# Performance work log

Measured on AMD Instinct MI355X. Metric: run time of the kernel, lower is better.

## Reference

```python
import jax, jax.numpy as jnp
import numpy as np

MARGIN = 0.1  # init kwarg


def setup_inputs() -> dict:
    key = jax.random.key(0)
    k1, k2, k3 = jax.random.split(key, 3)
    B, P, D = 256, 64, 1024
    imFtr = jax.random.normal(k1, (B, P, D), dtype=jnp.float32)
    disFtr = jax.random.normal(k2, (B, D), dtype=jnp.float32)
    lblList = jax.random.randint(k3, (B,), 0, 100000, dtype=jnp.int64 if jax.config.read('jax_enable_x64') else jnp.int32)
    return {"imFtr": imFtr, "disFtr": disFtr, "lblList": lblList}


def reference(imFtr, disFtr, lblList):
    B, P, D = imFtr.shape
    # simMM: [B*P, B] -> [B, P, B]; max over proposals P -> simMax [B, B]
    simMM = jnp.einsum('bpd,cd->bpc', imFtr, disFtr)
    simMax = jnp.max(simMM, axis=1)  # [B, B] (rows: image/video i, cols: text j)
    pos = jnp.diagonal(simMax)       # [B]

    # valid negative pairs: labels differ (diagonal excluded automatically)
    mask = (lblList[:, None] != lblList[None, :]).astype(simMax.dtype)  # [B, B]
    pairNum = jnp.sum(mask)

    # image -> text ranking: relu(sim[i, j] - sim[i, i] + margin)
    loss_it = jnp.sum(jnp.maximum(simMax - pos[:, None] + MARGIN, 0.0) * mask)
    loss = loss_it / pairNum

    # biLossFlag: text -> image ranking: relu(sim[j, i] - sim[i, i] + margin)
    loss_ti = jnp.sum(jnp.maximum(simMax - pos[None, :] + MARGIN, 0.0) * mask)
    loss = loss + jnp.where(pairNum > 0, loss_ti / pairNum, 0.0)

    return loss.reshape(1)
```

## Files before the change

### kernel.cpp

```cpp
#include <hip/hip_runtime.h>

constexpr int NB = 256;
constexpr int NP = 64;
constexpr int ND = 1024;
constexpr float MARGIN = 0.1f;

typedef __attribute__((ext_vector_type(8))) short bf16x8;
typedef __attribute__((ext_vector_type(4))) short bf16x4;
typedef __attribute__((ext_vector_type(4))) float f32x4;

static __device__ inline unsigned short f2bf(float f) {
  unsigned u = __builtin_bit_cast(unsigned, f);
  u += 0x7fffu + ((u >> 16) & 1u);
  return (unsigned short)(u >> 16);
}

static __device__ inline bf16x8 cvt8(float4 a, float4 b) {
  bf16x8 r;
  r[0] = (short)f2bf(a.x); r[1] = (short)f2bf(a.y);
  r[2] = (short)f2bf(a.z); r[3] = (short)f2bf(a.w);
  r[4] = (short)f2bf(b.x); r[5] = (short)f2bf(b.y);
  r[6] = (short)f2bf(b.z); r[7] = (short)f2bf(b.w);
  return r;
}

static __device__ inline bf16x4 cvt4(float4 a) {
  bf16x4 r;
  r[0] = (short)f2bf(a.x); r[1] = (short)f2bf(a.y);
  r[2] = (short)f2bf(a.z); r[3] = (short)f2bf(a.w);
  return r;
}

__global__ __launch_bounds__(256) void cvtB_kernel(
    const float* __restrict__ src, short* __restrict__ dst) {
  const int idx = (blockIdx.x * 256 + threadIdx.x) * 4;
  float4 v = *reinterpret_cast<const float4*>(src + idx);
  *reinterpret_cast<bf16x4*>(dst + idx) = cvt4(v);
}

__global__ __launch_bounds__(1024, 4) void simmax_kernel(
    const float* __restrict__ imFtr, const short* __restrict__ disB,
    float* __restrict__ simMax) {
  const int i  = blockIdx.x;
  const int t  = threadIdx.x;
  const int w  = t >> 6;
  const int l  = t & 63;
  const int lr = l & 15;
  const int lk = l >> 4;

  __shared__ short Asl[2][NP][256];

  f32x4 acc[4];
#pragma unroll
  for (int pt = 0; pt < 4; ++pt)
#pragma unroll
    for (int r = 0; r < 4; ++r) acc[pt][r] = 0.0f;

  const int ar = t >> 4;
  const int aj = t & 15;
  const float* abase = imFtr + ((size_t)i * NP + ar) * ND + aj * 4;
  float4 areg[4];

  const short* bp = disB + (size_t)(w * 16 + lr) * ND + lk * 8;
  bf16x8 breg[8];

#define STAGE_LOAD(C)                                                        \
  _Pragma("unroll")                                                          \
  for (int g = 0; g < 4; ++g)                                                \
    areg[g] = *reinterpret_cast<const float4*>(abase + (C) * 256 + g * 64);

#define STAGE_WRITE(BUF)                                                     \
  _Pragma("unroll")                                                          \
  for (int g = 0; g < 4; ++g) {                                              \
    const int s  = g * 8 + (aj >> 1);                                        \
    const int so = (s ^ (ar & 15)) * 8 + (aj & 1) * 4;                       \
    *reinterpret_cast<bf16x4*>(&Asl[BUF][ar][so]) = cvt4(areg[g]);           \
  }

  STAGE_LOAD(0);
#pragma unroll
  for (int j = 0; j < 8; ++j)
    breg[j] = *reinterpret_cast<const bf16x8*>(bp + j * 32);
  STAGE_WRITE(0);
  __syncthreads();

#pragma unroll
  for (int c = 0; c < 4; ++c) {
    const int cb = c & 1;
    if (c < 3) STAGE_LOAD(c + 1);
#pragma unroll
    for (int j8 = 0; j8 < 8; ++j8) {
      const int jj = c * 8 + j8;
      const int so = ((j8 * 4 + lk) ^ lr) * 8;
      bf16x8 a0 = *reinterpret_cast<const bf16x8*>(&Asl[cb][lr][so]);
      bf16x8 a1 = *reinterpret_cast<const bf16x8*>(&Asl[cb][16 + lr][so]);
      bf16x8 a2 = *reinterpret_cast<const bf16x8*>(&Asl[cb][32 + lr][so]);
      bf16x8 a3 = *reinterpret_cast<const bf16x8*>(&Asl[cb][48 + lr][so]);
      acc[0] = __builtin_amdgcn_mfma_f32_16x16x32_bf16(a0, breg[j8], acc[0], 0, 0, 0);
      acc[1] = __builtin_amdgcn_mfma_f32_16x16x32_bf16(a1, breg[j8], acc[1], 0, 0, 0);
      acc[2] = __builtin_amdgcn_mfma_f32_16x16x32_bf16(a2, breg[j8], acc[2], 0, 0, 0);
      acc[3] = __builtin_amdgcn_mfma_f32_16x16x32_bf16(a3, breg[j8], acc[3], 0, 0, 0);
      if (jj + 8 < 32)
        breg[j8] = *reinterpret_cast<const bf16x8*>(bp + (jj + 8) * 32);
    }
    if (c < 3) {
      STAGE_WRITE(cb ^ 1);
      __syncthreads();
    }
  }

#undef STAGE_LOAD
#undef STAGE_WRITE

  float m = acc[0][0];
#pragma unroll
  for (int pt = 0; pt < 4; ++pt)
#pragma unroll
    for (int r = 0; r < 4; ++r) m = fmaxf(m, acc[pt][r]);
  m = fmaxf(m, __shfl_xor(m, 16));
  m = fmaxf(m, __shfl_xor(m, 32));
  if (l < 16) simMax[(size_t)i * NB + w * 16 + lr] = m;
}

__global__ __launch_bounds__(512) void simmax_fallback_kernel(
    const float* __restrict__ imFtr, const float* __restrict__ disFtr,
    float* __restrict__ simMax) {
  const int i  = blockIdx.x;
  const int t  = threadIdx.x;
  const int w  = t >> 6;
  const int l  = t & 63;
  const int lr = l & 15;
  const int lk = l >> 4;

  __shared__ short Asl[NP][64];

  f32x4 acc[4][2];
#pragma unroll
  for (int pt = 0; pt < 4; ++pt)
#pragma unroll
    for (int ct = 0; ct < 2; ++ct)
#pragma unroll
      for (int r = 0; r < 4; ++r) acc[pt][ct][r] = 0.0f;

  const int ar  = t >> 3;
  const int aks = t & 7;
  const float* ap = imFtr + (size_t)i * NP * ND + (size_t)ar * ND + aks * 8;
  const int wslot = ((aks ^ (ar & 7)) * 8);
  float4 av0 = *reinterpret_cast<const float4*>(ap);
  float4 av1 = *reinterpret_cast<const float4*>(ap + 4);

  const float* bp0 = disFtr + (size_t)(w * 32 + lr) * ND + lk * 8;
  const float* bp1 = disFtr + (size_t)(w * 32 + 16 + lr) * ND + lk * 8;

  for (int kc = 0; kc < 16; ++kc) {
    const int kbase = kc * 64;
    float4 bld[2][2][2];
#pragma unroll
    for (int ks = 0; ks < 2; ++ks) {
      const int ko = kbase + ks * 32;
      bld[ks][0][0] = *reinterpret_cast<const float4*>(bp0 + ko);
      bld[ks][0][1] = *reinterpret_cast<const float4*>(bp0 + ko + 4);
      bld[ks][1][0] = *reinterpret_cast<const float4*>(bp1 + ko);
      bld[ks][1][1] = *reinterpret_cast<const float4*>(bp1 + ko + 4);
    }
    __syncthreads();
    *reinterpret_cast<bf16x8*>(&Asl[ar][wslot]) = cvt8(av0, av1);
    if (kc < 15) {
      const float* apn = ap + (kc + 1) * 64;
      av0 = *reinterpret_cast<const float4*>(apn);
      av1 = *reinterpret_cast<const float4*>(apn + 4);
    }
    __syncthreads();

#pragma unroll
    for (int ks = 0; ks < 2; ++ks) {
      bf16x8 bfr0 = cvt8(bld[ks][0][0], bld[ks][0][1]);
      bf16x8 bfr1 = cvt8(bld[ks][1][0], bld[ks][1][1]);
#pragma unroll
      for (int pt = 0; pt < 4; ++pt) {
        const int row  = pt * 16 + lr;
        const int slot = (((ks * 4 + lk) ^ (row & 7)) * 8);
        bf16x8 afr = *reinterpret_cast<const bf16x8*>(&Asl[row][slot]);
        acc[pt][0] = __builtin_amdgcn_mfma_f32_16x16x32_bf16(afr, bfr0, acc[pt][0], 0, 0, 0);
        acc[pt][1] = __builtin_amdgcn_mfma_f32_16x16x32_bf16(afr, bfr1, acc[pt][1], 0, 0, 0);
      }
    }
  }

#pragma unroll
  for (int ct = 0; ct < 2; ++ct) {
    float m = acc[0][ct][0];
#pragma unroll
    for (int pt = 0; pt < 4; ++pt)
#pragma unroll
      for (int r = 0; r < 4; ++r) m = fmaxf(m, acc[pt][ct][r]);
    m = fmaxf(m, __shfl_xor(m, 16));
    m = fmaxf(m, __shfl_xor(m, 32));
    if (l < 16) simMax[(size_t)i * NB + w * 32 + ct * 16 + l] = m;
  }
}

__global__ __launch_bounds__(256) void loss_kernel(
    const float* __restrict__ simMax, const int* __restrict__ lbl,
    float* __restrict__ partial) {
  const int i = blockIdx.x;
  const int j = threadIdx.x;
  __shared__ float posi_sh;
  __shared__ float red[3][4];

  float s = simMax[(size_t)i * NB + j];
  if (j == i) posi_sh = s;
  __syncthreads();
  const float posi = posi_sh;
  const float posj = simMax[(size_t)j * NB + j];

  const float msk = (lbl[i] != lbl[j]) ? 1.0f : 0.0f;
  float c  = msk;
  float l1 = msk * fmaxf(s - posi + MARGIN, 0.0f);
  float l2 = msk * fmaxf(s - posj + MARGIN, 0.0f);
#pragma unroll
  for (int o = 32; o > 0; o >>= 1) {
    c  += __shfl_down(c, o);
    l1 += __shfl_down(l1, o);
    l2 += __shfl_down(l2, o);
  }
  const int w = j >> 6;
  if ((j & 63) == 0) { red[0][w] = c; red[1][w] = l1; red[2][w] = l2; }
  __syncthreads();
  if (j == 0) {
    partial[i * 3 + 0] = red[0][0] + red[0][1] + red[0][2] + red[0][3];
    partial[i * 3 + 1] = red[1][0] + red[1][1] + red[1][2] + red[1][3];
    partial[i * 3 + 2] = red[2][0] + red[2][1] + red[2][2] + red[2][3];
  }
}

__global__ __launch_bounds__(256) void finalize_kernel(
    const float* __restrict__ partial, float* __restrict__ out) {
  const int t = threadIdx.x;
  __shared__ float red[3][4];
  float c  = partial[t * 3 + 0];
  float l1 = partial[t * 3 + 1];
  float l2 = partial[t * 3 + 2];
#pragma unroll
  for (int o = 32; o > 0; o >>= 1) {
    c  += __shfl_down(c, o);
    l1 += __shfl_down(l1, o);
    l2 += __shfl_down(l2, o);
  }
  const int w = t >> 6;
  if ((t & 63) == 0) { red[0][w] = c; red[1][w] = l1; red[2][w] = l2; }
  __syncthreads();
  if (t == 0) {
    float cs  = red[0][0] + red[0][1] + red[0][2] + red[0][3];
    float l1s = red[1][0] + red[1][1] + red[1][2] + red[1][3];
    float l2s = red[2][0] + red[2][1] + red[2][2] + red[2][3];
    float loss = l1s / cs;
    loss += (cs > 0.0f) ? (l2s / cs) : 0.0f;
    out[0] = loss;
  }
}

extern "C" void kernel_launch(void* const* d_in, const int* in_sizes, int n_in,
                              void* d_out, int out_size, void* d_ws, size_t ws_size,
                              hipStream_t stream) {
  (void)in_sizes; (void)n_in; (void)out_size;
  const float* imFtr  = (const float*)d_in[0];
  const float* disFtr = (const float*)d_in[1];
  const int*   lbl    = (const int*)d_in[2];
  float* out = (float*)d_out;

  const size_t disB_bytes = (size_t)NB * ND * sizeof(short);
  const size_t sim_bytes  = (size_t)NB * NB * sizeof(float);
  const size_t need = disB_bytes + sim_bytes + 3 * NB * sizeof(float);

  if (ws_size >= need) {
    short* disB    = (short*)d_ws;
    float* simMax  = (float*)((char*)d_ws + disB_bytes);
    float* partial = (float*)((char*)d_ws + disB_bytes + sim_bytes);

    cvtB_kernel<<<dim3(NB), dim3(256), 0, stream>>>(disFtr, disB);
    simmax_kernel<<<dim3(NB), dim3(1024), 0, stream>>>(imFtr, disB, simMax);
    loss_kernel<<<dim3(NB), dim3(256), 0, stream>>>(simMax, lbl, partial);
    finalize_kernel<<<dim3(1), dim3(256), 0, stream>>>(partial, out);
  } else {
    float* simMax  = (float*)d_ws;
    float* partial = (float*)((char*)d_ws + (size_t)NB * NB * 4);
    simmax_fallback_kernel<<<dim3(NB), dim3(512), 0, stream>>>(imFtr, disFtr, simMax);
    loss_kernel<<<dim3(NB), dim3(256), 0, stream>>>(simMax, lbl, partial);
    finalize_kernel<<<dim3(1), dim3(256), 0, stream>>>(partial, out);
  }
}
```

Before: 34.48 us.

## Fuse conversion, simMax GEMM and loss reductions into one cooperative kernel

Replaces four separate launches (bf16 conversion, simMax GEMM, per-row loss, finalize) with a single cooperative kernel that uses grid.sync between phases. The goal is to remove launch gaps and kernel boundaries on a short pipeline. In exchange it adds three grid-wide barriers and depends on all 256 blocks of 1024 threads being co-resident. It also drops the workspace-size fallback path. The first A-tile prefetch is issued before the conversion phase so its latency overlaps the first barrier.

```diff
diff --git a/kernel.cpp b/kernel.cpp
--- a/kernel.cpp
+++ b/kernel.cpp
@@ -1,4 +1,7 @@
 #include <hip/hip_runtime.h>
+#include <hip/hip_cooperative_groups.h>
+
+namespace cg = cooperative_groups;
 
 constexpr int NB = 256;
 constexpr int NP = 64;
@@ -13,15 +16,6 @@
   unsigned u = __builtin_bit_cast(unsigned, f);
   u += 0x7fffu + ((u >> 16) & 1u);
   return (unsigned short)(u >> 16);
-}
-
-static __device__ inline bf16x8 cvt8(float4 a, float4 b) {
-  bf16x8 r;
-  r[0] = (short)f2bf(a.x); r[1] = (short)f2bf(a.y);
-  r[2] = (short)f2bf(a.z); r[3] = (short)f2bf(a.w);
-  r[4] = (short)f2bf(b.x); r[5] = (short)f2bf(b.y);
-  r[6] = (short)f2bf(b.z); r[7] = (short)f2bf(b.w);
-  return r;
 }
 
 static __device__ inline bf16x4 cvt4(float4 a) {
@@ -31,16 +25,13 @@
   return r;
 }
 
-__global__ __launch_bounds__(256) void cvtB_kernel(
-    const float* __restrict__ src, short* __restrict__ dst) {
-  const int idx = (blockIdx.x * 256 + threadIdx.x) * 4;
-  float4 v = *reinterpret_cast<const float4*>(src + idx);
-  *reinterpret_cast<bf16x4*>(dst + idx) = cvt4(v);
-}
-
-__global__ __launch_bounds__(1024, 4) void simmax_kernel(
-    const float* __restrict__ imFtr, const short* __restrict__ disB,
-    float* __restrict__ simMax) {
+__global__ __launch_bounds__(1024, 4) void fused_kernel(
+    const float* __restrict__ imFtr, const float* __restrict__ disFtr,
+    const int* __restrict__ lbl, float* __restrict__ out,
+    short* __restrict__ disB, float* __restrict__ simMax,
+    float* __restrict__ partial) {
+  cg::grid_group grid = cg::this_grid();
+
   const int i  = blockIdx.x;
   const int t  = threadIdx.x;
   const int w  = t >> 6;
@@ -49,20 +40,13 @@
   const int lk = l >> 4;
 
   __shared__ short Asl[2][NP][256];
-
-  f32x4 acc[4];
-#pragma unroll
-  for (int pt = 0; pt < 4; ++pt)
-#pragma unroll
-    for (int r = 0; r < 4; ++r) acc[pt][r] = 0.0f;
+  __shared__ float red_sh[3][4];
+  __shared__ float posi_sh;
 
   const int ar = t >> 4;
   const int aj = t & 15;
   const float* abase = imFtr + ((size_t)i * NP + ar) * ND + aj * 4;
   float4 areg[4];
-
-  const short* bp = disB + (size_t)(w * 16 + lr) * ND + lk * 8;
-  bf16x8 breg[8];
 
 #define STAGE_LOAD(C)                                                        \
   _Pragma("unroll")                                                          \
@@ -78,192 +62,137 @@
   }
 
   STAGE_LOAD(0);
-#pragma unroll
-  for (int j = 0; j < 8; ++j)
-    breg[j] = *reinterpret_cast<const bf16x8*>(bp + j * 32);
-  STAGE_WRITE(0);
-  __syncthreads();
-
-#pragma unroll
-  for (int c = 0; c < 4; ++c) {
-    const int cb = c & 1;
-    if (c < 3) STAGE_LOAD(c + 1);
-#pragma unroll
-    for (int j8 = 0; j8 < 8; ++j8) {
-      const int jj = c * 8 + j8;
-      const int so = ((j8 * 4 + lk) ^ lr) * 8;
-      bf16x8 a0 = *reinterpret_cast<const bf16x8*>(&Asl[cb][lr][so]);
-      bf16x8 a1 = *reinterpret_cast<const bf16x8*>(&Asl[cb][16 + lr][so]);
-      bf16x8 a2 = *reinterpret_cast<const bf16x8*>(&Asl[cb][32 + lr][so]);
-      bf16x8 a3 = *reinterpret_cast<const bf16x8*>(&Asl[cb][48 + lr][so]);
-      acc[0] = __builtin_amdgcn_mfma_f32_16x16x32_bf16(a0, breg[j8], acc[0], 0, 0, 0);
-      acc[1] = __builtin_amdgcn_mfma_f32_16x16x32_bf16(a1, breg[j8], acc[1], 0, 0, 0);
-      acc[2] = __builtin_amdgcn_mfma_f32_16x16x32_bf16(a2, breg[j8], acc[2], 0, 0, 0);
-      acc[3] = __builtin_amdgcn_mfma_f32_16x16x32_bf16(a3, breg[j8], acc[3], 0, 0, 0);
-      if (jj + 8 < 32)
-        breg[j8] = *reinterpret_cast<const bf16x8*>(bp + (jj + 8) * 32);
-    }
-    if (c < 3) {
-      STAGE_WRITE(cb ^ 1);
-      __syncthreads();
-    }
-  }
-
+  {
+    const int gid = i * 1024 + t;
+    if (gid < (NB * ND) / 4) {
+      const int idx = gid * 4;
+      float4 v = *reinterpret_cast<const float4*>(disFtr + idx);
+      *reinterpret_cast<bf16x4*>(disB + idx) = cvt4(v);
+    }
+  }
+  grid.sync();
+
+  {
+    f32x4 acc[4];
+#pragma unroll
+    for (int pt = 0; pt < 4; ++pt)
+#pragma unroll
+      for (int r = 0; r < 4; ++r) acc[pt][r] = 0.0f;
+
+    const short* bp = disB + (size_t)(w * 16 + lr) * ND + lk * 8;
+    bf16x8 breg[8];
+#pragma unroll
+    for (int j = 0; j < 8; ++j)
+      breg[j] = *reinterpret_cast<const bf16x8*>(bp + j * 32);
+
+    STAGE_WRITE(0);
+    __syncthreads();
+
+#pragma unroll
+    for (int c = 0; c < 4; ++c) {
+      const int cb = c & 1;
+      if (c < 3) STAGE_LOAD(c + 1);
+#pragma unroll
+      for (int j8 = 0; j8 < 8; ++j8) {
+        const int jj = c * 8 + j8;
+        const int so = ((j8 * 4 + lk) ^ lr) * 8;
+        bf16x8 a0 = *reinterpret_cast<const bf16x8*>(&Asl[cb][lr][so]);
+        bf16x8 a1 = *reinterpret_cast<const bf16x8*>(&Asl[cb][16 + lr][so]);
+        bf16x8 a2 = *reinterpret_cast<const bf16x8*>(&Asl[cb][32 + lr][so]);
+        bf16x8 a3 = *reinterpret_cast<const bf16x8*>(&Asl[cb][48 + lr][so]);
+        acc[0] = __builtin_amdgcn_mfma_f32_16x16x32_bf16(a0, breg[j8], acc[0], 0, 0, 0);
+        acc[1] = __builtin_amdgcn_mfma_f32_16x16x32_bf16(a1, breg[j8], acc[1], 0, 0, 0);
+        acc[2] = __builtin_amdgcn_mfma_f32_16x16x32_bf16(a2, breg[j8], acc[2], 0, 0, 0);
+        acc[3] = __builtin_amdgcn_mfma_f32_16x16x32_bf16(a3, breg[j8], acc[3], 0, 0, 0);
+        if (jj + 8 < 32)
+          breg[j8] = *reinterpret_cast<const bf16x8*>(bp + (jj + 8) * 32);
+      }
+      if (c < 3) {
+        STAGE_WRITE(cb ^ 1);
+        __syncthreads();
+      }
+    }
+
+    float m = acc[0][0];
+#pragma unroll
+    for (int pt = 0; pt < 4; ++pt)
+#pragma unroll
+      for (int r = 0; r < 4; ++r) m = fmaxf(m, acc[pt][r]);
+    m = fmaxf(m, __shfl_xor(m, 16));
+    m = fmaxf(m, __shfl_xor(m, 32));
+    if (l < 16) simMax[(size_t)i * NB + w * 16 + lr] = m;
+  }
 #undef STAGE_LOAD
 #undef STAGE_WRITE
-
-  float m = acc[0][0];
-#pragma unroll
-  for (int pt = 0; pt < 4; ++pt)
-#pragma unroll
-    for (int r = 0; r < 4; ++r) m = fmaxf(m, acc[pt][r]);
-  m = fmaxf(m, __shfl_xor(m, 16));
-  m = fmaxf(m, __shfl_xor(m, 32));
-  if (l < 16) simMax[(size_t)i * NB + w * 16 + lr] = m;
-}
-
-__global__ __launch_bounds__(512) void simmax_fallback_kernel(
-    const float* __restrict__ imFtr, const float* __restrict__ disFtr,
-    float* __restrict__ simMax) {
-  const int i  = blockIdx.x;
-  const int t  = threadIdx.x;
-  const int w  = t >> 6;
-  const int l  = t & 63;
-  const int lr = l & 15;
-  const int lk = l >> 4;
-
-  __shared__ short Asl[NP][64];
-
-  f32x4 acc[4][2];
-#pragma unroll
-  for (int pt = 0; pt < 4; ++pt)
-#pragma unroll
-    for (int ct = 0; ct < 2; ++ct)
-#pragma unroll
-      for (int r = 0; r < 4; ++r) acc[pt][ct][r] = 0.0f;
-
-  const int ar  = t >> 3;
-  const int aks = t & 7;
-  const float* ap = imFtr + (size_t)i * NP * ND + (size_t)ar * ND + aks * 8;
-  const int wslot = ((aks ^ (ar & 7)) * 8);
-  float4 av0 = *reinterpret_cast<const float4*>(ap);
-  float4 av1 = *reinterpret_cast<const float4*>(ap + 4);
-
-  const float* bp0 = disFtr + (size_t)(w * 32 + lr) * ND + lk * 8;
-  const float* bp1 = disFtr + (size_t)(w * 32 + 16 + lr) * ND + lk * 8;
-
-  for (int kc = 0; kc < 16; ++kc) {
-    const int kbase = kc * 64;
-    float4 bld[2][2][2];
-#pragma unroll
-    for (int ks = 0; ks < 2; ++ks) {
-      const int ko = kbase + ks * 32;
-      bld[ks][0][0] = *reinterpret_cast<const float4*>(bp0 + ko);
-      bld[ks][0][1] = *reinterpret_cast<const float4*>(bp0 + ko + 4);
-      bld[ks][1][0] = *reinterpret_cast<const float4*>(bp1 + ko);
-      bld[ks][1][1] = *reinterpret_cast<const float4*>(bp1 + ko + 4);
-    }
-    __syncthreads();
-    *reinterpret_cast<bf16x8*>(&Asl[ar][wslot]) = cvt8(av0, av1);
-    if (kc < 15) {
-      const float* apn = ap + (kc + 1) * 64;
-      av0 = *reinterpret_cast<const float4*>(apn);
-      av1 = *reinterpret_cast<const float4*>(apn + 4);
-    }
-    __syncthreads();
-
-#pragma unroll
-    for (int ks = 0; ks < 2; ++ks) {
-      bf16x8 bfr0 = cvt8(bld[ks][0][0], bld[ks][0][1]);
-      bf16x8 bfr1 = cvt8(bld[ks][1][0], bld[ks][1][1]);
-#pragma unroll
-      for (int pt = 0; pt < 4; ++pt) {
-        const int row  = pt * 16 + lr;
-        const int slot = (((ks * 4 + lk) ^ (row & 7)) * 8);
-        bf16x8 afr = *reinterpret_cast<const bf16x8*>(&Asl[row][slot]);
-        acc[pt][0] = __builtin_amdgcn_mfma_f32_16x16x32_bf16(afr, bfr0, acc[pt][0], 0, 0, 0);
-        acc[pt][1] = __builtin_amdgcn_mfma_f32_16x16x32_bf16(afr, bfr1, acc[pt][1], 0, 0, 0);
-      }
-    }
-  }
-
-#pragma unroll
-  for (int ct = 0; ct < 2; ++ct) {
-    float m = acc[0][ct][0];
-#pragma unroll
-    for (int pt = 0; pt < 4; ++pt)
-#pragma unroll
-      for (int r = 0; r < 4; ++r) m = fmaxf(m, acc[pt][ct][r]);
-    m = fmaxf(m, __shfl_xor(m, 16));
-    m = fmaxf(m, __shfl_xor(m, 32));
-    if (l < 16) simMax[(size_t)i * NB + w * 32 + ct * 16 + l] = m;
-  }
-}
-
-__global__ __launch_bounds__(256) void loss_kernel(
-    const float* __restrict__ simMax, const int* __restrict__ lbl,
-    float* __restrict__ partial) {
-  const int i = blockIdx.x;
-  const int j = threadIdx.x;
-  __shared__ float posi_sh;
-  __shared__ float red[3][4];
-
-  float s = simMax[(size_t)i * NB + j];
-  if (j == i) posi_sh = s;
-  __syncthreads();
-  const float posi = posi_sh;
-  const float posj = simMax[(size_t)j * NB + j];
-
-  const float msk = (lbl[i] != lbl[j]) ? 1.0f : 0.0f;
-  float c  = msk;
-  float l1 = msk * fmaxf(s - posi + MARGIN, 0.0f);
-  float l2 = msk * fmaxf(s - posj + MARGIN, 0.0f);
-#pragma unroll
-  for (int o = 32; o > 0; o >>= 1) {
-    c  += __shfl_down(c, o);
-    l1 += __shfl_down(l1, o);
-    l2 += __shfl_down(l2, o);
-  }
-  const int w = j >> 6;
-  if ((j & 63) == 0) { red[0][w] = c; red[1][w] = l1; red[2][w] = l2; }
-  __syncthreads();
-  if (j == 0) {
-    partial[i * 3 + 0] = red[0][0] + red[0][1] + red[0][2] + red[0][3];
-    partial[i * 3 + 1] = red[1][0] + red[1][1] + red[1][2] + red[1][3];
-    partial[i * 3 + 2] = red[2][0] + red[2][1] + red[2][2] + red[2][3];
-  }
-}
-
-__global__ __launch_bounds__(256) void finalize_kernel(
-    const float* __restrict__ partial, float* __restrict__ out) {
-  const int t = threadIdx.x;
-  __shared__ float red[3][4];
-  float c  = partial[t * 3 + 0];
-  float l1 = partial[t * 3 + 1];
-  float l2 = partial[t * 3 + 2];
-#pragma unroll
-  for (int o = 32; o > 0; o >>= 1) {
-    c  += __shfl_down(c, o);
-    l1 += __shfl_down(l1, o);
-    l2 += __shfl_down(l2, o);
-  }
-  const int w = t >> 6;
-  if ((t & 63) == 0) { red[0][w] = c; red[1][w] = l1; red[2][w] = l2; }
-  __syncthreads();
-  if (t == 0) {
-    float cs  = red[0][0] + red[0][1] + red[0][2] + red[0][3];
-    float l1s = red[1][0] + red[1][1] + red[1][2] + red[1][3];
-    float l2s = red[2][0] + red[2][1] + red[2][2] + red[2][3];
-    float loss = l1s / cs;
-    loss += (cs > 0.0f) ? (l2s / cs) : 0.0f;
-    out[0] = loss;
+  grid.sync();
+
+  {
+    const int j = t;
+    float s = 0.0f, posj = 0.0f, msk = 0.0f;
+    if (j < NB) {
+      s = simMax[(size_t)i * NB + j];
+      if (j == i) posi_sh = s;
+      posj = simMax[(size_t)j * NB + j];
+      msk = (lbl[i] != lbl[j]) ? 1.0f : 0.0f;
+    }
+    __syncthreads();
+    float c = 0.0f, l1 = 0.0f, l2 = 0.0f;
+    if (j < NB) {
+      const float posi = posi_sh;
+      c  = msk;
+      l1 = msk * fmaxf(s - posi + MARGIN, 0.0f);
+      l2 = msk * fmaxf(s - posj + MARGIN, 0.0f);
+    }
+#pragma unroll
+    for (int o = 32; o > 0; o >>= 1) {
+      c  += __shfl_down(c, o);
+      l1 += __shfl_down(l1, o);
+      l2 += __shfl_down(l2, o);
+    }
+    if (j < NB && (j & 63) == 0) {
+      red_sh[0][j >> 6] = c; red_sh[1][j >> 6] = l1; red_sh[2][j >> 6] = l2;
+    }
+    __syncthreads();
+    if (j == 0) {
+      partial[i * 3 + 0] = red_sh[0][0] + red_sh[0][1] + red_sh[0][2] + red_sh[0][3];
+      partial[i * 3 + 1] = red_sh[1][0] + red_sh[1][1] + red_sh[1][2] + red_sh[1][3];
+      partial[i * 3 + 2] = red_sh[2][0] + red_sh[2][1] + red_sh[2][2] + red_sh[2][3];
+    }
+  }
+  grid.sync();
+
+  if (i == 0) {
+    float c = 0.0f, l1 = 0.0f, l2 = 0.0f;
+    if (t < NB) {
+      c  = partial[t * 3 + 0];
+      l1 = partial[t * 3 + 1];
+      l2 = partial[t * 3 + 2];
+    }
+#pragma unroll
+    for (int o = 32; o > 0; o >>= 1) {
+      c  += __shfl_down(c, o);
+      l1 += __shfl_down(l1, o);
+      l2 += __shfl_down(l2, o);
+    }
+    if (t < NB && (t & 63) == 0) {
+      red_sh[0][t >> 6] = c; red_sh[1][t >> 6] = l1; red_sh[2][t >> 6] = l2;
+    }
+    __syncthreads();
+    if (t == 0) {
+      float cs  = red_sh[0][0] + red_sh[0][1] + red_sh[0][2] + red_sh[0][3];
+      float l1s = red_sh[1][0] + red_sh[1][1] + red_sh[1][2] + red_sh[1][3];
+      float l2s = red_sh[2][0] + red_sh[2][1] + red_sh[2][2] + red_sh[2][3];
+      float loss = l1s / cs;
+      loss += (cs > 0.0f) ? (l2s / cs) : 0.0f;
+      out[0] = loss;
+    }
   }
 }
 
 extern "C" void kernel_launch(void* const* d_in, const int* in_sizes, int n_in,
                               void* d_out, int out_size, void* d_ws, size_t ws_size,
                               hipStream_t stream) {
-  (void)in_sizes; (void)n_in; (void)out_size;
+  (void)in_sizes; (void)n_in; (void)out_size; (void)ws_size;
   const float* imFtr  = (const float*)d_in[0];
   const float* disFtr = (const float*)d_in[1];
   const int*   lbl    = (const int*)d_in[2];
@@ -271,22 +200,13 @@
 
   const size_t disB_bytes = (size_t)NB * ND * sizeof(short);
   const size_t sim_bytes  = (size_t)NB * NB * sizeof(float);
-  const size_t need = disB_bytes + sim_bytes + 3 * NB * sizeof(float);
-
-  if (ws_size >= need) {
-    short* disB    = (short*)d_ws;
-    float* simMax  = (float*)((char*)d_ws + disB_bytes);
-    float* partial = (float*)((char*)d_ws + disB_bytes + sim_bytes);
-
-    cvtB_kernel<<<dim3(NB), dim3(256), 0, stream>>>(disFtr, disB);
-    simmax_kernel<<<dim3(NB), dim3(1024), 0, stream>>>(imFtr, disB, simMax);
-    loss_kernel<<<dim3(NB), dim3(256), 0, stream>>>(simMax, lbl, partial);
-    finalize_kernel<<<dim3(1), dim3(256), 0, stream>>>(partial, out);
-  } else {
-    float* simMax  = (float*)d_ws;
-    float* partial = (float*)((char*)d_ws + (size_t)NB * NB * 4);
-    simmax_fallback_kernel<<<dim3(NB), dim3(512), 0, stream>>>(imFtr, disFtr, simMax);
-    loss_kernel<<<dim3(NB), dim3(256), 0, stream>>>(simMax, lbl, partial);
-    finalize_kernel<<<dim3(1), dim3(256), 0, stream>>>(partial, out);
-  }
-}
+
+  short* disB    = (short*)d_ws;
+  float* simMax  = (float*)((char*)d_ws + disB_bytes);
+  float* partial = (float*)((char*)d_ws + disB_bytes + sim_bytes);
+
+  void* args[] = {(void*)&imFtr, (void*)&disFtr, (void*)&lbl, (void*)&out,
+                  (void*)&disB, (void*)&simMax, (void*)&partial};
+  hipLaunchCooperativeKernel((const void*)fused_kernel, dim3(NB), dim3(1024),
+                             args, 0, stream);
+}
```

Result: slower. 123.4 us (+257.9%).
